# Kernel tuning notes

Hardware: AMD Instinct MI355X
Metric: run time of the kernel (lower is better)

The kernel has to match this reference:

```python
import jax, jax.numpy as jnp
import numpy as np

EMBED = 1024
HEADS = 16
HEAD_DIM = EMBED // HEADS
B, T = 2, 2048
ROPE_THETA = 10000.0


def _rope(x):
    # x: [B, H, T, D]; standard half-split rotary embedding, applied per head
    D = x.shape[-1]
    inv_freq = 1.0 / (ROPE_THETA ** (jnp.arange(0, D, 2, dtype=jnp.float32) / D))  # [D/2]
    freqs = jnp.arange(x.shape[2], dtype=jnp.float32)[:, None] * inv_freq[None, :]  # [T, D/2]
    cos = jnp.cos(freqs).astype(x.dtype)  # [T, D/2]
    sin = jnp.sin(freqs).astype(x.dtype)
    x1, x2 = x[..., : D // 2], x[..., D // 2 :]
    return jnp.concatenate([x1 * cos - x2 * sin, x2 * cos + x1 * sin], axis=-1)


def setup_inputs() -> dict:
    key = jax.random.key(0)
    ks = jax.random.split(key, 5)
    s = 1.0 / np.sqrt(EMBED)
    return {
        "x": jax.random.normal(ks[0], (B, T, EMBED), dtype=jnp.float32),
        "Wq": jax.random.normal(ks[1], (EMBED, EMBED), dtype=jnp.float32) * s,
        "bq": jnp.zeros((EMBED,), dtype=jnp.float32),
        "Wk": jax.random.normal(ks[2], (EMBED, EMBED), dtype=jnp.float32) * s,
        "bk": jnp.zeros((EMBED,), dtype=jnp.float32),
        "Wv": jax.random.normal(ks[3], (EMBED, EMBED), dtype=jnp.float32) * s,
        "bv": jnp.zeros((EMBED,), dtype=jnp.float32),
        "Wo": jax.random.normal(ks[4], (EMBED, EMBED), dtype=jnp.float32) * s,
        "bo": jnp.zeros((EMBED,), dtype=jnp.float32),
    }


def reference(x, Wq, bq, Wk, bk, Wv, bv, Wo, bo):
    Bb, Tt, C = x.shape
    H, D = HEADS, HEAD_DIM
    # torch Linear: y = x @ W.T + b
    def proj(W, b):
        return (jnp.einsum("btc,oc->bto", x, W) + b).reshape(Bb, Tt, H, D).transpose(0, 2, 1, 3)

    q = _rope(proj(Wq, bq))  # [B, H, T, D]
    k = _rope(proj(Wk, bk))
    v = proj(Wv, bv)
    scale = jnp.sqrt(jnp.asarray(D, dtype=x.dtype))
    scores = jnp.einsum("bhtd,bhsd->bhts", q, k) / scale  # [B, H, T, T]
    attn = jax.nn.softmax(scores, axis=-1)  # dropout = identity in eval mode
    out = jnp.einsum("bhts,bhsd->bhtd", attn, v)  # [B, H, T, D]
    out = out.transpose(0, 2, 1, 3).reshape(Bb, Tt, C)
    return jnp.einsum("btc,oc->bto", out, Wo) + bo
```

## Files before the change

### kernel.cpp

```cpp
#include <hip/hip_runtime.h>
#include <hip/hip_bf16.h>

#define EMBED 1024
#define HEADS 16
#define HDIM 64
#define BATCH 2
#define SEQ 2048
#define MTOT (BATCH*SEQ)

typedef __attribute__((ext_vector_type(2))) float f32x2;
typedef __attribute__((ext_vector_type(4))) float f32x4;
typedef __attribute__((ext_vector_type(16))) float f32x16;
typedef __attribute__((ext_vector_type(4))) short s16x4;
typedef __attribute__((ext_vector_type(8))) short bf16x8;
typedef __attribute__((ext_vector_type(4))) int i32x4;

static __device__ __forceinline__ short f2bf(float f) {
  unsigned u = __builtin_bit_cast(unsigned, f);
  unsigned r = (u + 0x7fffu + ((u >> 16) & 1u)) >> 16;
  return (short)r;
}
static __device__ __forceinline__ float bf2f(short s) {
  unsigned u = ((unsigned)(unsigned short)s) << 16;
  return __builtin_bit_cast(float, u);
}
static __device__ __forceinline__ int pack2bf_fast(float lo, float hi) {
  unsigned ulo = __builtin_bit_cast(unsigned, lo) + 0x8000u;
  unsigned uhi = __builtin_bit_cast(unsigned, hi) + 0x8000u;
  int r;
  asm("v_cvt_pk_bf16_f32 %0, %1, %2" : "=v"(r)
      : "v"(__builtin_bit_cast(float, ulo)), "v"(__builtin_bit_cast(float, uhi)));
  return r;
}
static __device__ __forceinline__ void pswap(int &a, int &b) {
  asm("v_permlane32_swap_b32 %0, %1" : "+v"(a), "+v"(b));
}

typedef __attribute__((address_space(1))) const void gvoid_t;
typedef __attribute__((address_space(3))) void lvoid_t;
static __device__ __forceinline__ void gload_lds16(const void* g, void* l) {
  __builtin_amdgcn_global_load_lds((gvoid_t*)g, (lvoid_t*)l, 16, 0, 0);
}

__global__ __launch_bounds__(256) void cvt_bf16(
    const float* __restrict__ x,
    const float* __restrict__ Wq, const float* __restrict__ Wk,
    const float* __restrict__ Wv, const float* __restrict__ Wo,
    short* __restrict__ xb,
    short* __restrict__ Wqb, short* __restrict__ Wkb,
    short* __restrict__ Wvb, short* __restrict__ Wob,
    f32x2* __restrict__ tab)
{
  int i = blockIdx.x * 256 + threadIdx.x;
  if (i >= 2097152) {
    int i2 = i - 2097152;
    int t = i2 >> 5, j = i2 & 31;
    float invf = exp2f(-(float)j * 0.4152410118609203f);
    float sn, cs;
    sincosf((float)t * invf, &sn, &cs);
    f32x2 e; e[0] = cs; e[1] = sn;
    tab[i2] = e;
    return;
  }
  const float* src; short* dst; int off;
  if (i < 1048576) { src = x; dst = xb; off = i; }
  else {
    int j = i - 1048576;
    int w = j >> 18; off = j & 262143;
    src = (w == 0) ? Wq : (w == 1) ? Wk : (w == 2) ? Wv : Wo;
    dst = (w == 0) ? Wqb : (w == 1) ? Wkb : (w == 2) ? Wvb : Wob;
  }
  f32x4 v = ((const f32x4*)src)[off];
  s16x4 h;
#pragma unroll
  for (int j = 0; j < 4; ++j) h[j] = f2bf(v[j]);
  ((s16x4*)dst)[off] = h;
}

__global__ __launch_bounds__(256) void qkv_gemm(
    const short* __restrict__ xb,
    const short* __restrict__ Wqb, const short* __restrict__ Wkb, const short* __restrict__ Wvb,
    const float* __restrict__ bq, const float* __restrict__ bk, const float* __restrict__ bv,
    const f32x2* __restrict__ tab,
    short* __restrict__ Qb, short* __restrict__ Kb, short* __restrict__ Vb)
{
  __shared__ short As[128][64];
  __shared__ short Bs[128][64];
  int tid = threadIdx.x;
  int lane = tid & 63, wid = tid >> 6;
  int wm = wid >> 1, wn = wid & 1;
  int bm = blockIdx.x / 24;
  int bncol = blockIdx.x % 24;
  int wsel = bncol >> 3, bnn = bncol & 7;
  const short* W    = (wsel == 0) ? Wqb : (wsel == 1) ? Wkb : Wvb;
  const float* bias = (wsel == 0) ? bq : (wsel == 1) ? bk : bv;

  f32x4 acc[4][4] = {};

  const short* Abase = xb + (size_t)bm * 128 * EMBED;
  const short* Bbase = W + (size_t)bnn * 128 * EMBED;
  char* AsB = (char*)&As[0][0];
  char* BsB = (char*)&Bs[0][0];

  for (int kt = 0; kt < EMBED / 64; ++kt) {
#pragma unroll
    for (int i = 0; i < 4; ++i) {
      int s = tid + i * 256;
      int row = s >> 3, c = s & 7;
      int cs = c ^ (row & 7);
      gload_lds16(&Abase[(size_t)row * EMBED + kt * 64 + cs * 8],
                  AsB + i * 4096 + wid * 1024 + lane * 16);
      gload_lds16(&Bbase[(size_t)row * EMBED + kt * 64 + cs * 8],
                  BsB + i * 4096 + wid * 1024 + lane * 16);
    }
    __syncthreads();
#pragma unroll
    for (int kk = 0; kk < 2; ++kk) {
      int cp = ((kk * 4 + (lane >> 4)) ^ (lane & 7)) * 8;
      bf16x8 af[4], bfr[4];
#pragma unroll
      for (int mf = 0; mf < 4; ++mf)
        af[mf] = *(const bf16x8*)&As[wm * 64 + mf * 16 + (lane & 15)][cp];
#pragma unroll
      for (int nf = 0; nf < 4; ++nf)
        bfr[nf] = *(const bf16x8*)&Bs[wn * 64 + nf * 16 + (lane & 15)][cp];
      if (wsel == 2) {
#pragma unroll
        for (int mf = 0; mf < 4; ++mf)
#pragma unroll
          for (int nf = 0; nf < 4; ++nf)
            acc[mf][nf] = __builtin_amdgcn_mfma_f32_16x16x32_bf16(bfr[mf], af[nf], acc[mf][nf], 0, 0, 0);
      } else {
#pragma unroll
        for (int mf = 0; mf < 4; ++mf)
#pragma unroll
          for (int nf = 0; nf < 4; ++nf)
            acc[mf][nf] = __builtin_amdgcn_mfma_f32_16x16x32_bf16(af[mf], bfr[nf], acc[mf][nf], 0, 0, 0);
      }
    }
    __syncthreads();
  }

  if (wsel < 2) {
    short* dst = (wsel == 0) ? Qb : Kb;
    float sc = (wsel == 0) ? 0.18033688011112042f : 1.0f;
#pragma unroll
    for (int nf = 0; nf < 2; ++nf) {
      int col = bnn * 128 + wn * 64 + nf * 16 + (lane & 15);
      int h = col >> 6, j = col & 31;
      float b1 = bias[col], b2 = bias[col + 32];
#pragma unroll
      for (int mf = 0; mf < 4; ++mf) {
        int row0 = bm * 128 + wm * 64 + mf * 16 + ((lane >> 4) << 2);
#pragma unroll
        for (int r = 0; r < 4; ++r) {
          int m = row0 + r;
          int b_ = m >> 11, t = m & (SEQ - 1);
          f32x2 e = tab[t * 32 + j];
          float a1 = acc[mf][nf][r] + b1;
          float a2 = acc[mf][nf + 2][r] + b2;
          size_t o = (((size_t)(b_ * HEADS + h)) * SEQ + t) * HDIM + j;
          dst[o]      = f2bf((a1 * e[0] - a2 * e[1]) * sc);
          dst[o + 32] = f2bf((a2 * e[0] + a1 * e[1]) * sc);
        }
      }
    }
  } else {
#pragma unroll
    for (int mf = 0; mf < 4; ++mf) {
#pragma unroll
      for (int r = 0; r < 4; ++r) {
        int cch = bnn * 128 + wn * 64 + mf * 16 + ((lane >> 4) << 2) + r;
        int h = cch >> 6, d = cch & 63;
        float bb = bias[cch];
#pragma unroll
        for (int nf = 0; nf < 4; ++nf) {
          int m = bm * 128 + wm * 64 + nf * 16 + (lane & 15);
          int b_ = m >> 11, t = m & (SEQ - 1);
          Vb[((size_t)(b_ * HEADS + h) * HDIM + d) * SEQ + t] = f2bf(acc[mf][nf][r] + bb);
        }
      }
    }
  }
}

#define QBLK 128
#define KBLK 128

__global__ __launch_bounds__(256, 2) void attn_kernel(
    const short* __restrict__ Qb, const short* __restrict__ Kb,
    const short* __restrict__ Vb, short* __restrict__ Ob)
{
  __shared__ short Ks[KBLK][68];
  __shared__ short Vs[HDIM][132];

  int tid = threadIdx.x, lane = tid & 63, wid = tid >> 6;
  int l31 = lane & 31, lhi = lane >> 5;

  int bid = blockIdx.x;
  int swz = (bid & 7) * 64 + (bid >> 3);
  int qi = swz & 15, bh = swz >> 4;
  int b = bh >> 4, h = bh & 15;

  const short* Qp = Qb + ((size_t)bh * SEQ + qi * QBLK + wid * 32) * HDIM;
  const short* Kp = Kb + (size_t)bh * SEQ * HDIM;
  const short* Vp = Vb + (size_t)bh * HDIM * SEQ;

  bf16x8 qf[4];
#pragma unroll
  for (int cc = 0; cc < 4; ++cc)
    qf[cc] = *(const bf16x8*)&Qp[(size_t)l31 * HDIM + cc * 16 + lhi * 8];

  f32x16 oacc0 = {}, oacc1 = {}, lacc = {};
  bf16x8 vones;
#pragma unroll
  for (int j = 0; j < 8; ++j) vones[j] = (short)0x3F80;

  bf16x8 kreg[4], vreg[4];
#pragma unroll
  for (int i = 0; i < 4; ++i) {
    int s = tid + i * 256;
    kreg[i] = *(const bf16x8*)&Kp[(size_t)(s >> 3) * HDIM + (s & 7) * 8];
    vreg[i] = *(const bf16x8*)&Vp[(size_t)(s >> 4) * SEQ + (s & 15) * 8];
  }

  for (int kt = 0; kt < SEQ / KBLK; ++kt) {
#pragma unroll
    for (int i = 0; i < 4; ++i) {
      int s = tid + i * 256;
      *(bf16x8*)&Ks[s >> 3][(s & 7) * 8] = kreg[i];
      *(bf16x8*)&Vs[s >> 4][(s & 15) * 8] = vreg[i];
    }
    __syncthreads();

    if (kt + 1 < SEQ / KBLK) {
#pragma unroll
      for (int i = 0; i < 4; ++i) {
        int s = tid + i * 256;
        kreg[i] = *(const bf16x8*)&Kp[(size_t)((kt + 1) * KBLK + (s >> 3)) * HDIM + (s & 7) * 8];
        vreg[i] = *(const bf16x8*)&Vp[(size_t)(s >> 4) * SEQ + (kt + 1) * KBLK + (s & 15) * 8];
      }
    }

#pragma unroll
    for (int kbp = 0; kbp < 4; kbp += 2) {
      f32x16 s0 = {}, s1 = {};
#pragma unroll
      for (int cc = 0; cc < 4; ++cc) {
        bf16x8 a0 = *(const bf16x8*)&Ks[(kbp + 0) * 32 + l31][cc * 16 + lhi * 8];
        bf16x8 a1 = *(const bf16x8*)&Ks[(kbp + 1) * 32 + l31][cc * 16 + lhi * 8];
        s0 = __builtin_amdgcn_mfma_f32_32x32x16_bf16(a0, qf[cc], s0, 0, 0, 0);
        s1 = __builtin_amdgcn_mfma_f32_32x32x16_bf16(a1, qf[cc], s1, 0, 0, 0);
      }
      f32x16 p0, p1;
#pragma unroll
      for (int i = 0; i < 16; ++i) {
        p0[i] = __builtin_amdgcn_exp2f(s0[i]);
        p1[i] = __builtin_amdgcn_exp2f(s1[i]);
      }

#pragma unroll
      for (int c = 0; c < 2; ++c) {
        int w0 = pack2bf_fast(p0[8 * c + 0], p0[8 * c + 1]);
        int w1 = pack2bf_fast(p0[8 * c + 2], p0[8 * c + 3]);
        int w2 = pack2bf_fast(p0[8 * c + 4], p0[8 * c + 5]);
        int w3 = pack2bf_fast(p0[8 * c + 6], p0[8 * c + 7]);
        pswap(w0, w2);
        pswap(w1, w3);
        i32x4 pw; pw[0] = w0; pw[1] = w1; pw[2] = w2; pw[3] = w3;
        bf16x8 pa = __builtin_bit_cast(bf16x8, pw);

        bf16x8 vf0 = *(const bf16x8*)&Vs[l31][(kbp + 0) * 32 + c * 16 + lhi * 8];
        bf16x8 vf1 = *(const bf16x8*)&Vs[32 + l31][(kbp + 0) * 32 + c * 16 + lhi * 8];
        lacc = __builtin_amdgcn_mfma_f32_32x32x16_bf16(pa, vones, lacc, 0, 0, 0);
        oacc0 = __builtin_amdgcn_mfma_f32_32x32x16_bf16(pa, vf0, oacc0, 0, 0, 0);
        oacc1 = __builtin_amdgcn_mfma_f32_32x32x16_bf16(pa, vf1, oacc1, 0, 0, 0);
      }
#pragma unroll
      for (int c = 0; c < 2; ++c) {
        int w0 = pack2bf_fast(p1[8 * c + 0], p1[8 * c + 1]);
        int w1 = pack2bf_fast(p1[8 * c + 2], p1[8 * c + 3]);
        int w2 = pack2bf_fast(p1[8 * c + 4], p1[8 * c + 5]);
        int w3 = pack2bf_fast(p1[8 * c + 6], p1[8 * c + 7]);
        pswap(w0, w2);
        pswap(w1, w3);
        i32x4 pw; pw[0] = w0; pw[1] = w1; pw[2] = w2; pw[3] = w3;
        bf16x8 pa = __builtin_bit_cast(bf16x8, pw);

        bf16x8 vf0 = *(const bf16x8*)&Vs[l31][(kbp + 1) * 32 + c * 16 + lhi * 8];
        bf16x8 vf1 = *(const bf16x8*)&Vs[32 + l31][(kbp + 1) * 32 + c * 16 + lhi * 8];
        lacc = __builtin_amdgcn_mfma_f32_32x32x16_bf16(pa, vones, lacc, 0, 0, 0);
        oacc0 = __builtin_amdgcn_mfma_f32_32x32x16_bf16(pa, vf0, oacc0, 0, 0, 0);
        oacc1 = __builtin_amdgcn_mfma_f32_32x32x16_bf16(pa, vf1, oacc1, 0, 0, 0);
      }
    }
    __syncthreads();
  }

#pragma unroll
  for (int r = 0; r < 16; ++r) {
    int qrow = (r & 3) + 8 * (r >> 2) + 4 * lhi;
    int t = qi * QBLK + wid * 32 + qrow;
    float inv = 1.0f / lacc[r];
    size_t base = ((size_t)(b * SEQ + t)) * EMBED + h * HDIM;
    Ob[base + l31]      = f2bf(oacc0[r] * inv);
    Ob[base + 32 + l31] = f2bf(oacc1[r] * inv);
  }
}

__global__ __launch_bounds__(256) void out_gemm(
    const short* __restrict__ A, const short* __restrict__ Wob,
    const float* __restrict__ bo, float* __restrict__ C)
{
  __shared__ short As[128][64];
  __shared__ short Bs[128][64];
  int tid = threadIdx.x;
  int lane = tid & 63, wid = tid >> 6;
  int wm = wid >> 1, wn = wid & 1;
  int bm = blockIdx.x >> 3, bn = blockIdx.x & 7;

  f32x4 acc[4][4] = {};
  const short* Abase = A + (size_t)bm * 128 * EMBED;
  const short* Bbase = Wob + (size_t)bn * 128 * EMBED;
  char* AsB = (char*)&As[0][0];
  char* BsB = (char*)&Bs[0][0];

  for (int kt = 0; kt < EMBED / 64; ++kt) {
#pragma unroll
    for (int i = 0; i < 4; ++i) {
      int s = tid + i * 256;
      int row = s >> 3, c = s & 7;
      int cs = c ^ (row & 7);
      gload_lds16(&Abase[(size_t)row * EMBED + kt * 64 + cs * 8],
                  AsB + i * 4096 + wid * 1024 + lane * 16);
      gload_lds16(&Bbase[(size_t)row * EMBED + kt * 64 + cs * 8],
                  BsB + i * 4096 + wid * 1024 + lane * 16);
    }
    __syncthreads();
#pragma unroll
    for (int kk = 0; kk < 2; ++kk) {
      int cp = ((kk * 4 + (lane >> 4)) ^ (lane & 7)) * 8;
      bf16x8 af[4], bfr[4];
#pragma unroll
      for (int mf = 0; mf < 4; ++mf)
        af[mf] = *(const bf16x8*)&As[wm * 64 + mf * 16 + (lane & 15)][cp];
#pragma unroll
      for (int nf = 0; nf < 4; ++nf)
        bfr[nf] = *(const bf16x8*)&Bs[wn * 64 + nf * 16 + (lane & 15)][cp];
#pragma unroll
      for (int mf = 0; mf < 4; ++mf)
#pragma unroll
        for (int nf = 0; nf < 4; ++nf)
          acc[mf][nf] = __builtin_amdgcn_mfma_f32_16x16x32_bf16(af[mf], bfr[nf], acc[mf][nf], 0, 0, 0);
    }
    __syncthreads();
  }

#pragma unroll
  for (int nf = 0; nf < 4; ++nf) {
    int col = bn * 128 + wn * 64 + nf * 16 + (lane & 15);
    float bb = bo[col];
#pragma unroll
    for (int mf = 0; mf < 4; ++mf) {
      int row0 = bm * 128 + wm * 64 + mf * 16 + ((lane >> 4) << 2);
#pragma unroll
      for (int r = 0; r < 4; ++r)
        C[(size_t)(row0 + r) * EMBED + col] = acc[mf][nf][r] + bb;
    }
  }
}

extern "C" void kernel_launch(void* const* d_in, const int* in_sizes, int n_in,
                              void* d_out, int out_size, void* d_ws, size_t ws_size,
                              hipStream_t stream) {
  const float* x  = (const float*)d_in[0];
  const float* Wq = (const float*)d_in[1];
  const float* bq = (const float*)d_in[2];
  const float* Wk = (const float*)d_in[3];
  const float* bk = (const float*)d_in[4];
  const float* Wv = (const float*)d_in[5];
  const float* bv = (const float*)d_in[6];
  const float* Wo = (const float*)d_in[7];
  const float* bo = (const float*)d_in[8];
  float* out = (float*)d_out;
  char* ws = (char*)d_ws;

  const size_t MB = 1u << 20;
  short* Qb  = (short*)(ws);
  short* Kb  = (short*)(ws + 8 * MB);
  short* Vb  = (short*)(ws + 16 * MB);
  short* XOb = (short*)(ws + 24 * MB);
  short* Wqb = (short*)(ws + 32 * MB);
  short* Wkb = (short*)(ws + 34 * MB);
  short* Wvb = (short*)(ws + 36 * MB);
  short* Wob = (short*)(ws + 38 * MB);
  f32x2* tab = (f32x2*)(ws + 40 * MB);

  cvt_bf16<<<dim3(8448), dim3(256), 0, stream>>>(x, Wq, Wk, Wv, Wo, XOb, Wqb, Wkb, Wvb, Wob, tab);
  qkv_gemm<<<dim3(32 * 24), dim3(256), 0, stream>>>(XOb, Wqb, Wkb, Wvb, bq, bk, bv, tab, Qb, Kb, Vb);
  attn_kernel<<<dim3(BATCH * HEADS * (SEQ / QBLK)), dim3(256), 0, stream>>>(Qb, Kb, Vb, XOb);
  out_gemm<<<dim3(32 * 8), dim3(256), 0, stream>>>(XOb, Wob, bo, out);
}
```

Before: 121.7 us.

## Add MFMA wave priority in attention and shrink out-GEMM M-tile to 64

Wraps the QK^T and PV MFMA sequences in the attention kernel with s_setprio so waves issuing matrix ops get scheduling priority over waves doing exp/pack work. Separately, the output projection GEMM now uses 64x128 tiles with each wave owning a 16-row strip, doubling the grid to 512 blocks so more of the 256 CUs get work. The smaller tile lowers reuse of the weight tile per block and increases B-tile loads from global memory.

```diff
diff --git a/kernel.cpp b/kernel.cpp
--- a/kernel.cpp
+++ b/kernel.cpp
@@ -245,6 +245,7 @@
 #pragma unroll
     for (int kbp = 0; kbp < 4; kbp += 2) {
       f32x16 s0 = {}, s1 = {};
+      __builtin_amdgcn_s_setprio(1);
 #pragma unroll
       for (int cc = 0; cc < 4; ++cc) {
         bf16x8 a0 = *(const bf16x8*)&Ks[(kbp + 0) * 32 + l31][cc * 16 + lhi * 8];
@@ -252,6 +253,7 @@
         s0 = __builtin_amdgcn_mfma_f32_32x32x16_bf16(a0, qf[cc], s0, 0, 0, 0);
         s1 = __builtin_amdgcn_mfma_f32_32x32x16_bf16(a1, qf[cc], s1, 0, 0, 0);
       }
+      __builtin_amdgcn_s_setprio(0);
       f32x16 p0, p1;
 #pragma unroll
       for (int i = 0; i < 16; ++i) {
@@ -272,9 +274,11 @@
 
         bf16x8 vf0 = *(const bf16x8*)&Vs[l31][(kbp + 0) * 32 + c * 16 + lhi * 8];
         bf16x8 vf1 = *(const bf16x8*)&Vs[32 + l31][(kbp + 0) * 32 + c * 16 + lhi * 8];
+        __builtin_amdgcn_s_setprio(1);
         lacc = __builtin_amdgcn_mfma_f32_32x32x16_bf16(pa, vones, lacc, 0, 0, 0);
         oacc0 = __builtin_amdgcn_mfma_f32_32x32x16_bf16(pa, vf0, oacc0, 0, 0, 0);
         oacc1 = __builtin_amdgcn_mfma_f32_32x32x16_bf16(pa, vf1, oacc1, 0, 0, 0);
+        __builtin_amdgcn_s_setprio(0);
       }
 #pragma unroll
       for (int c = 0; c < 2; ++c) {
@@ -289,9 +293,11 @@
 
         bf16x8 vf0 = *(const bf16x8*)&Vs[l31][(kbp + 1) * 32 + c * 16 + lhi * 8];
         bf16x8 vf1 = *(const bf16x8*)&Vs[32 + l31][(kbp + 1) * 32 + c * 16 + lhi * 8];
+        __builtin_amdgcn_s_setprio(1);
         lacc = __builtin_amdgcn_mfma_f32_32x32x16_bf16(pa, vones, lacc, 0, 0, 0);
         oacc0 = __builtin_amdgcn_mfma_f32_32x32x16_bf16(pa, vf0, oacc0, 0, 0, 0);
         oacc1 = __builtin_amdgcn_mfma_f32_32x32x16_bf16(pa, vf1, oacc1, 0, 0, 0);
+        __builtin_amdgcn_s_setprio(0);
       }
     }
     __syncthreads();
@@ -312,27 +318,32 @@
     const short* __restrict__ A, const short* __restrict__ Wob,
     const float* __restrict__ bo, float* __restrict__ C)
 {
-  __shared__ short As[128][64];
+  __shared__ short As[64][64];
   __shared__ short Bs[128][64];
   int tid = threadIdx.x;
   int lane = tid & 63, wid = tid >> 6;
-  int wm = wid >> 1, wn = wid & 1;
   int bm = blockIdx.x >> 3, bn = blockIdx.x & 7;
 
-  f32x4 acc[4][4] = {};
-  const short* Abase = A + (size_t)bm * 128 * EMBED;
+  f32x4 acc[8] = {};
+  const short* Abase = A + (size_t)bm * 64 * EMBED;
   const short* Bbase = Wob + (size_t)bn * 128 * EMBED;
   char* AsB = (char*)&As[0][0];
   char* BsB = (char*)&Bs[0][0];
 
   for (int kt = 0; kt < EMBED / 64; ++kt) {
 #pragma unroll
-    for (int i = 0; i < 4; ++i) {
+    for (int i = 0; i < 2; ++i) {
       int s = tid + i * 256;
       int row = s >> 3, c = s & 7;
       int cs = c ^ (row & 7);
       gload_lds16(&Abase[(size_t)row * EMBED + kt * 64 + cs * 8],
                   AsB + i * 4096 + wid * 1024 + lane * 16);
+    }
+#pragma unroll
+    for (int i = 0; i < 4; ++i) {
+      int s = tid + i * 256;
+      int row = s >> 3, c = s & 7;
+      int cs = c ^ (row & 7);
       gload_lds16(&Bbase[(size_t)row * EMBED + kt * 64 + cs * 8],
                   BsB + i * 4096 + wid * 1024 + lane * 16);
     }
@@ -340,33 +351,24 @@
 #pragma unroll
     for (int kk = 0; kk < 2; ++kk) {
       int cp = ((kk * 4 + (lane >> 4)) ^ (lane & 7)) * 8;
-      bf16x8 af[4], bfr[4];
-#pragma unroll
-      for (int mf = 0; mf < 4; ++mf)
-        af[mf] = *(const bf16x8*)&As[wm * 64 + mf * 16 + (lane & 15)][cp];
-#pragma unroll
-      for (int nf = 0; nf < 4; ++nf)
-        bfr[nf] = *(const bf16x8*)&Bs[wn * 64 + nf * 16 + (lane & 15)][cp];
-#pragma unroll
-      for (int mf = 0; mf < 4; ++mf)
-#pragma unroll
-        for (int nf = 0; nf < 4; ++nf)
-          acc[mf][nf] = __builtin_amdgcn_mfma_f32_16x16x32_bf16(af[mf], bfr[nf], acc[mf][nf], 0, 0, 0);
-    }
-    __syncthreads();
-  }
-
-#pragma unroll
-  for (int nf = 0; nf < 4; ++nf) {
-    int col = bn * 128 + wn * 64 + nf * 16 + (lane & 15);
+      bf16x8 af = *(const bf16x8*)&As[wid * 16 + (lane & 15)][cp];
+#pragma unroll
+      for (int nf = 0; nf < 8; ++nf) {
+        bf16x8 bfr = *(const bf16x8*)&Bs[nf * 16 + (lane & 15)][cp];
+        acc[nf] = __builtin_amdgcn_mfma_f32_16x16x32_bf16(af, bfr, acc[nf], 0, 0, 0);
+      }
+    }
+    __syncthreads();
+  }
+
+#pragma unroll
+  for (int nf = 0; nf < 8; ++nf) {
+    int col = bn * 128 + nf * 16 + (lane & 15);
     float bb = bo[col];
-#pragma unroll
-    for (int mf = 0; mf < 4; ++mf) {
-      int row0 = bm * 128 + wm * 64 + mf * 16 + ((lane >> 4) << 2);
-#pragma unroll
-      for (int r = 0; r < 4; ++r)
-        C[(size_t)(row0 + r) * EMBED + col] = acc[mf][nf][r] + bb;
-    }
+    int row0 = bm * 64 + wid * 16 + ((lane >> 4) << 2);
+#pragma unroll
+    for (int r = 0; r < 4; ++r)
+      C[(size_t)(row0 + r) * EMBED + col] = acc[nf][r] + bb;
   }
 }
 
@@ -399,5 +401,5 @@
   cvt_bf16<<<dim3(8448), dim3(256), 0, stream>>>(x, Wq, Wk, Wv, Wo, XOb, Wqb, Wkb, Wvb, Wob, tab);
   qkv_gemm<<<dim3(32 * 24), dim3(256), 0, stream>>>(XOb, Wqb, Wkb, Wvb, bq, bk, bv, tab, Qb, Kb, Vb);
   attn_kernel<<<dim3(BATCH * HEADS * (SEQ / QBLK)), dim3(256), 0, stream>>>(Qb, Kb, Vb, XOb);
-  out_gemm<<<dim3(32 * 8), dim3(256), 0, stream>>>(XOb, Wob, bo, out);
-}
+  out_gemm<<<dim3(64 * 8), dim3(256), 0, stream>>>(XOb, Wob, bo, out);
+}
```

Measured after the change: 121.0 us. Within noise of the previous version (-0.6%).
